# Performance work log

Hardware: AMD Instinct MI355X
Metric: run time of the kernel (lower is better)

## Reference

```python
import jax, jax.numpy as jnp
import numpy as np

B, S, D = 4, 2048, 1024   # batch, seq_len, input feature dim
H, E = 16, 64             # head_num, att_embedding_size; H*E = model dim


def setup_inputs() -> dict:
    key = jax.random.key(0)
    ks = jax.random.split(key, 9)
    std = 1.0 / np.sqrt(D)
    M = H * E
    return {
        "x": jax.random.normal(ks[0], (B, S, D), dtype=jnp.float32),
        "Wq": jax.random.normal(ks[1], (D, M), dtype=jnp.float32) * std,
        "bq": jnp.zeros((M,), dtype=jnp.float32),
        "Wk": jax.random.normal(ks[2], (D, M), dtype=jnp.float32) * std,
        "bk": jnp.zeros((M,), dtype=jnp.float32),
        "Wv": jax.random.normal(ks[3], (D, M), dtype=jnp.float32) * std,
        "bv": jnp.zeros((M,), dtype=jnp.float32),
        "Wr": jax.random.normal(ks[4], (D, M), dtype=jnp.float32) * std,
        "br": jnp.zeros((M,), dtype=jnp.float32),
    }


def reference(x, Wq, bq, Wk, bk, Wv, bv, Wr, br):
    # QKV dense layers with ReLU activation (as in the original Keras code)
    qw = jax.nn.relu(x @ Wq + bq)                      # [B,S,H*E]
    kw = jax.nn.relu(x @ Wk + bk)
    vw = jax.nn.relu(x @ Wv + bv)
    # split heads: [B,S,H,E] -> [B,H,S,E]
    qw = qw.reshape(B, S, H, E).transpose(0, 2, 1, 3)
    kw = kw.reshape(B, S, H, E).transpose(0, 2, 1, 3)
    vw = vw.reshape(B, S, H, E).transpose(0, 2, 1, 3)
    # unscaled attention (original has no 1/sqrt(d) scaling)
    a = jnp.einsum("bhqe,bhke->bhqk", qw, kw)          # [B,H,S,S]
    a = jax.nn.softmax(a, axis=-1)
    o = jnp.einsum("bhqk,bhke->bhqe", a, vw)           # [B,H,S,E]
    o = o.transpose(0, 2, 1, 3).reshape(B, S, H * E)
    # residual dense (no activation)
    o = o + (x @ Wr + br)
    return o
```

## Files before the change

### kernel.cpp

```cpp
#include <hip/hip_runtime.h>


typedef __bf16 bf16x8 __attribute__((ext_vector_type(8)));
typedef float  f32x4  __attribute__((ext_vector_type(4)));
typedef short  short8 __attribute__((ext_vector_type(8)));
typedef short  short4v __attribute__((ext_vector_type(4)));
typedef float  float4v __attribute__((ext_vector_type(4)));
typedef int    int4v  __attribute__((ext_vector_type(4)));

#define LOG2E 1.44269504088896f

__device__ __forceinline__ unsigned short f2bf(float f) {
  unsigned u = __builtin_bit_cast(unsigned, f);
  u += 0x7fffu + ((u >> 16) & 1u);
  return (unsigned short)(u >> 16);
}

__device__ __forceinline__ unsigned pack2(float lo, float hi) {
  __bf16 a = (__bf16)lo, b = (__bf16)hi;
  unsigned short ua = __builtin_bit_cast(unsigned short, a);
  unsigned short ub = __builtin_bit_cast(unsigned short, b);
  return (unsigned)ua | ((unsigned)ub << 16);
}

__global__ __launch_bounds__(256) void k_cvt_x(const float* __restrict__ x,
                                               short* __restrict__ Xb) {
  const size_t i = ((size_t)blockIdx.x * 256 + threadIdx.x) * 4;
  float4v f = *(const float4v*)(x + i);
  short4v o;
  o[0] = (short)f2bf(f[0]); o[1] = (short)f2bf(f[1]);
  o[2] = (short)f2bf(f[2]); o[3] = (short)f2bf(f[3]);
  *(short4v*)(Xb + i) = o;
}

__global__ __launch_bounds__(256) void k_cvt_w(const float* __restrict__ Wq,
                                               const float* __restrict__ Wk,
                                               const float* __restrict__ Wv,
                                               const float* __restrict__ Wr,
                                               short* __restrict__ Wc) {
  const int bid = blockIdx.x;
  const int w = bid >> 8;
  const int t = bid & 255;
  const int tr = t >> 4, tc = t & 15;
  const float* Ws = (w == 0) ? Wq : (w == 1) ? Wk : (w == 2) ? Wv : Wr;
  __shared__ float T[64][65];
  const int tx = threadIdx.x & 63, ty = threadIdx.x >> 6;
#pragma unroll
  for (int i = 0; i < 16; ++i)
    T[i * 4 + ty][tx] = Ws[(size_t)(tr * 64 + i * 4 + ty) * 1024 + tc * 64 + tx];
  __syncthreads();
#pragma unroll
  for (int i = 0; i < 16; ++i) {
    const int n = tc * 64 + i * 4 + ty;
    Wc[((size_t)w * 1024 + n) * 1024 + tr * 64 + tx] = (short)f2bf(T[tx][i * 4 + ty]);
  }
}

__global__ __launch_bounds__(256) void k_gemm(const short* __restrict__ Xb,
                                              const short* __restrict__ Wc,
                                              const float* __restrict__ bq,
                                              const float* __restrict__ bk2,
                                              const float* __restrict__ bv,
                                              const float* __restrict__ br,
                                              short* __restrict__ Qb,
                                              short* __restrict__ Kb,
                                              short* __restrict__ Vb,
                                              float* __restrict__ Out) {
  __shared__ short As[128 * 32];
  __shared__ short Bs[128 * 32];
  const int tid = threadIdx.x, wid = tid >> 6, lane = tid & 63;
  const int lr = lane & 15, hi = lane >> 4;
  const int bm = blockIdx.x & 63, bn = blockIdx.x >> 6;
  const int m0 = bm * 128, n0 = bn * 128;
  const int wr = wid >> 1, wc = wid & 1;

  f32x4 acc[4][4] = {};

  const int c0 = wid * 2;
  const int srow = lane >> 2;
  const int scol = (lane & 3) * 8;

  for (int k0 = 0; k0 < 1024; k0 += 32) {
    __syncthreads();
    const short* a0 = Xb + (size_t)(m0 + c0 * 16 + srow) * 1024 + k0 + scol;
    const short* a1 = Xb + (size_t)(m0 + (c0 + 1) * 16 + srow) * 1024 + k0 + scol;
    const short* b0 = Wc + (size_t)(n0 + c0 * 16 + srow) * 1024 + k0 + scol;
    const short* b1 = Wc + (size_t)(n0 + (c0 + 1) * 16 + srow) * 1024 + k0 + scol;
    __builtin_amdgcn_global_load_lds((const __attribute__((address_space(1))) void*)a0,
                                     (__attribute__((address_space(3))) void*)&As[c0 * 512], 16, 0, 0);
    __builtin_amdgcn_global_load_lds((const __attribute__((address_space(1))) void*)a1,
                                     (__attribute__((address_space(3))) void*)&As[(c0 + 1) * 512], 16, 0, 0);
    __builtin_amdgcn_global_load_lds((const __attribute__((address_space(1))) void*)b0,
                                     (__attribute__((address_space(3))) void*)&Bs[c0 * 512], 16, 0, 0);
    __builtin_amdgcn_global_load_lds((const __attribute__((address_space(1))) void*)b1,
                                     (__attribute__((address_space(3))) void*)&Bs[(c0 + 1) * 512], 16, 0, 0);
    __syncthreads();

    bf16x8 af[4], bfr[4];
#pragma unroll
    for (int i = 0; i < 4; ++i)
      af[i] = *(const bf16x8*)&As[(wr * 64 + i * 16 + lr) * 32 + hi * 8];
#pragma unroll
    for (int j = 0; j < 4; ++j)
      bfr[j] = *(const bf16x8*)&Bs[(wc * 64 + j * 16 + lr) * 32 + hi * 8];
#pragma unroll
    for (int i = 0; i < 4; ++i)
#pragma unroll
      for (int j = 0; j < 4; ++j)
        acc[i][j] = __builtin_amdgcn_mfma_f32_16x16x32_bf16(af[i], bfr[j], acc[i][j], 0, 0, 0);
  }

#pragma unroll
  for (int i = 0; i < 4; ++i) {
    const int mbase = m0 + wr * 64 + i * 16 + hi * 4;
#pragma unroll
    for (int j = 0; j < 4; ++j) {
      const int n = n0 + wc * 64 + j * 16 + lr;
      const float* bp = (n < 2048) ? (n < 1024 ? bq : bk2) : (n < 3072 ? bv : br);
      const float bias = bp[n & 1023];
#pragma unroll
      for (int r = 0; r < 4; ++r) {
        float v = acc[i][j][r] + bias;
        const int m = mbase + r;
        if (n < 3072) {
          v = fmaxf(v, 0.0f);
          const int which = n >> 10;
          const int nn = n & 1023, h = nn >> 6, e = nn & 63;
          short* dst = (which == 0) ? Qb : (which == 1) ? Kb : Vb;
          const int bb = m >> 11, ss = m & 2047;
          dst[(((size_t)bb * 16 + h) * 2048 + ss) * 64 + e] = (short)f2bf(v);
        } else {
          Out[(size_t)m * 1024 + (n - 3072)] = v;
        }
      }
    }
  }
}

__global__ __launch_bounds__(256) void k_tr_v(const short* __restrict__ Vb,
                                              short* __restrict__ Vt) {
  __shared__ short T[64][72];
  const int bh = blockIdx.x >> 5;
  const int s0 = (blockIdx.x & 31) * 64;
  const size_t base = (size_t)bh * 2048 * 64;
  const int t = threadIdx.x;
  const int sl = t >> 2, e0 = (t & 3) * 16;
  const short* src = Vb + base + (size_t)(s0 + sl) * 64 + e0;
  *(short8*)&T[sl][e0] = *(const short8*)src;
  *(short8*)&T[sl][e0 + 8] = *(const short8*)(src + 8);
  __syncthreads();
  const int el = t >> 2, sc0 = (t & 3) * 16;
  const int b32 = sc0 & ~31;
  const int s_off = sc0 & 31;
  short tmp[16];
#pragma unroll
  for (int j = 0; j < 16; ++j) {
    const int sig = s_off + j;
    const int key = ((sig & 4) ? 16 : 0) + ((sig >> 3) << 2) + (sig & 3);
    tmp[j] = T[b32 + key][el];
  }
  short* dst = Vt + base + (size_t)el * 2048 + s0 + sc0;
  *(short8*)dst = *(const short8*)&tmp[0];
  *(short8*)(dst + 8) = *(const short8*)&tmp[8];
}

__global__ __launch_bounds__(256, 4) void k_attn(const short* __restrict__ Qb,
                                                 const short* __restrict__ Kb,
                                                 const short* __restrict__ Vt,
                                                 float* __restrict__ Out) {
  __shared__ __align__(16) short smem[16384];
  char* const sb = (char*)smem;
  const int tid = threadIdx.x, wid = tid >> 6, lane = tid & 63;
  const int lr = lane & 15, hi = lane >> 4;
  const int bid = ((blockIdx.x & 7) << 7) | (blockIdx.x >> 3);
  const int bh = bid >> 4;
  const int q0 = (bid & 15) * 128;
  const size_t hb = (size_t)bh * (2048 * 64);

  bf16x8 aq[2][2];
#pragma unroll
  for (int g = 0; g < 2; ++g) {
    const short* qp = Qb + hb + (size_t)(q0 + wid * 32 + g * 16 + lr) * 64 + hi * 8;
    aq[g][0] = *(const bf16x8*)qp;
    aq[g][1] = *(const bf16x8*)(qp + 32);
  }

  f32x4 o[2][4] = {};
  float l_run[2] = {0.f, 0.f};

  const int swz = ((lane & 7) ^ (lane >> 3)) * 8;
  const int rlo = lane >> 3;
  const int wr0 = wid * 16;
  const short* kp0 = Kb + hb + (size_t)(wr0 + rlo) * 64 + swz;
  const short* kp1 = kp0 + 8 * 64;
  const short* vp0 = Vt + hb + (size_t)(wr0 + rlo) * 2048 + swz;
  const short* vp1 = vp0 + 8 * 2048;

  const int vb0 = (lr * 64 + ((hi ^ (lr & 7)) << 3)) * 2;
  const int vb1 = vb0 ^ 64;

#define GLL(SRC, LDSOFF)                                                                   \
  __builtin_amdgcn_global_load_lds((const __attribute__((address_space(1))) void*)(SRC),   \
      (__attribute__((address_space(3))) void*)(sb + (LDSOFF)), 16, 0, 0)

  GLL(kp0, wr0 * 128);
  GLL(kp1, wr0 * 128 + 1024);
  GLL(vp0, 16384 + wr0 * 128);
  GLL(vp1, 16384 + wr0 * 128 + 1024);
  kp0 += 4096; kp1 += 4096; vp0 += 64; vp1 += 64;

  for (int kt = 0; kt < 32; ++kt) {
    const int buf = kt & 1;
    if (kt < 31) {
      const int d = (buf ^ 1) * 8192 + wr0 * 128;
      GLL(kp0, d);
      GLL(kp1, d + 1024);
      GLL(vp0, 16384 + d);
      GLL(vp1, 16384 + d + 1024);
      kp0 += 4096; kp1 += 4096; vp0 += 64; vp1 += 64;
      asm volatile("s_waitcnt vmcnt(4)" ::: "memory");
    } else {
      asm volatile("s_waitcnt vmcnt(0)" ::: "memory");
    }
    __builtin_amdgcn_sched_barrier(0);
    __builtin_amdgcn_s_barrier();
    __builtin_amdgcn_sched_barrier(0);

    f32x4 s[2][4];
#pragma unroll
    for (int kc = 0; kc < 4; ++kc) {
      const bf16x8 kf0 = *(const bf16x8*)(sb + (vb0 + buf * 8192 + kc * 2048));
      const bf16x8 kf1 = *(const bf16x8*)(sb + (vb1 + buf * 8192 + kc * 2048));
      f32x4 t0 = __builtin_amdgcn_mfma_f32_16x16x32_bf16(kf0, aq[0][0], (f32x4){0.f, 0.f, 0.f, 0.f}, 0, 0, 0);
      s[0][kc] = __builtin_amdgcn_mfma_f32_16x16x32_bf16(kf1, aq[0][1], t0, 0, 0, 0);
      f32x4 t1 = __builtin_amdgcn_mfma_f32_16x16x32_bf16(kf0, aq[1][0], (f32x4){0.f, 0.f, 0.f, 0.f}, 0, 0, 0);
      s[1][kc] = __builtin_amdgcn_mfma_f32_16x16x32_bf16(kf1, aq[1][1], t1, 0, 0, 0);
    }

    int4v pw[2][2];
#pragma unroll
    for (int g = 0; g < 2; ++g) {
      float sum = 0.f;
#pragma unroll
      for (int kc = 0; kc < 4; ++kc) {
        const float p0 = __builtin_amdgcn_exp2f(s[g][kc][0] * LOG2E);
        const float p1 = __builtin_amdgcn_exp2f(s[g][kc][1] * LOG2E);
        const float p2 = __builtin_amdgcn_exp2f(s[g][kc][2] * LOG2E);
        const float p3 = __builtin_amdgcn_exp2f(s[g][kc][3] * LOG2E);
        sum += (p0 + p1) + (p2 + p3);
        pw[g][kc >> 1][(kc & 1) * 2] = (int)pack2(p0, p1);
        pw[g][kc >> 1][(kc & 1) * 2 + 1] = (int)pack2(p2, p3);
      }
      l_run[g] += sum;
    }

#pragma unroll
    for (int kk = 0; kk < 2; ++kk) {
      const bf16x8 pa0 = __builtin_bit_cast(bf16x8, pw[0][kk]);
      const bf16x8 pa1 = __builtin_bit_cast(bf16x8, pw[1][kk]);
      const int cb = (kk ? vb1 : vb0) + 16384 + buf * 8192;
#pragma unroll
      for (int et = 0; et < 4; ++et) {
        const bf16x8 vf = *(const bf16x8*)(sb + (cb + et * 2048));
        o[0][et] = __builtin_amdgcn_mfma_f32_16x16x32_bf16(vf, pa0, o[0][et], 0, 0, 0);
        o[1][et] = __builtin_amdgcn_mfma_f32_16x16x32_bf16(vf, pa1, o[1][et], 0, 0, 0);
      }
    }

    asm volatile("s_waitcnt lgkmcnt(0)" ::: "memory");
    __builtin_amdgcn_sched_barrier(0);
    __builtin_amdgcn_s_barrier();
    __builtin_amdgcn_sched_barrier(0);
  }

  float* Ep = (float*)smem + wid * 1088;
  const int b = bh >> 4, h = bh & 15;
  const int qr = lane >> 2, cc = lane & 3;
#pragma unroll
  for (int g = 0; g < 2; ++g) {
    float lt = l_run[g];
    lt += __shfl_xor(lt, 16);
    lt += __shfl_xor(lt, 32);
    const float inv = 1.0f / lt;
#pragma unroll
    for (int et = 0; et < 4; ++et) {
      f32x4 v = o[g][et] * inv;
      *(float4v*)&Ep[lr * 68 + et * 16 + hi * 4] = v;
    }
    asm volatile("s_waitcnt lgkmcnt(0)" ::: "memory");
    const size_t gb = ((size_t)b * 2048 + q0 + wid * 32 + g * 16 + qr) * 1024 + h * 64 + cc * 4;
#pragma unroll
    for (int i = 0; i < 4; ++i) {
      float4v v = *(const float4v*)&Ep[qr * 68 + cc * 4 + i * 16];
      float4v u = *(const float4v*)&Out[gb + i * 16];
      u += v;
      *(float4v*)&Out[gb + i * 16] = u;
    }
    asm volatile("s_waitcnt lgkmcnt(0)" ::: "memory");
  }
#undef GLL
}

extern "C" void kernel_launch(void* const* d_in, const int* in_sizes, int n_in,
                              void* d_out, int out_size, void* d_ws, size_t ws_size,
                              hipStream_t stream) {
  const float* x  = (const float*)d_in[0];
  const float* Wq = (const float*)d_in[1];
  const float* bq = (const float*)d_in[2];
  const float* Wk = (const float*)d_in[3];
  const float* bk = (const float*)d_in[4];
  const float* Wv = (const float*)d_in[5];
  const float* bv = (const float*)d_in[6];
  const float* Wr = (const float*)d_in[7];
  const float* br = (const float*)d_in[8];
  float* Out = (float*)d_out;

  char* ws = (char*)d_ws;
  short* Xb = (short*)(ws);
  short* Wc = (short*)(ws + (size_t)16 * 1024 * 1024);
  short* Qb = (short*)(ws + (size_t)24 * 1024 * 1024);
  short* Kb = (short*)(ws + (size_t)40 * 1024 * 1024);
  short* Vb = (short*)(ws + (size_t)56 * 1024 * 1024);
  short* Vt = (short*)(ws);

  k_cvt_x<<<8192, 256, 0, stream>>>(x, Xb);
  k_cvt_w<<<1024, 256, 0, stream>>>(Wq, Wk, Wv, Wr, Wc);
  k_gemm<<<2048, 256, 0, stream>>>(Xb, Wc, bq, bk, bv, br, Qb, Kb, Vb, Out);
  k_tr_v<<<2048, 256, 0, stream>>>(Vb, Vt);
  k_attn<<<1024, 256, 0, stream>>>(Qb, Kb, Vt, Out);
}
```

Before: 201.2 us.

## Fuse V transpose into GEMM epilogue and widen attention query tile

The GEMM epilogue now writes V directly in the transposed, key-permuted layout the attention kernel reads, so the separate transpose kernel and its extra read/write pass over V go away. The attention kernel now handles 256 query rows per block (64 per wave) instead of 128, so each K/V tile loaded into shared memory is reused by twice as many queries, and the grid halves to 512 blocks. MFMA sections are wrapped in s_setprio. In exchange, register pressure goes up (launch bounds drop to 2 blocks per CU), and the V stores from the GEMM become strided 8-byte scatters.

```diff
diff --git a/kernel.cpp b/kernel.cpp
--- a/kernel.cpp
+++ b/kernel.cpp
@@ -7,6 +7,7 @@
 typedef short  short4v __attribute__((ext_vector_type(4)));
 typedef float  float4v __attribute__((ext_vector_type(4)));
 typedef int    int4v  __attribute__((ext_vector_type(4)));
+typedef unsigned uint2v __attribute__((ext_vector_type(2)));
 
 #define LOG2E 1.44269504088896f
 
@@ -64,7 +65,7 @@
                                               const float* __restrict__ br,
                                               short* __restrict__ Qb,
                                               short* __restrict__ Kb,
-                                              short* __restrict__ Vb,
+                                              short* __restrict__ Vt,
                                               float* __restrict__ Out) {
   __shared__ short As[128 * 32];
   __shared__ short Bs[128 * 32];
@@ -113,58 +114,40 @@
 #pragma unroll
   for (int i = 0; i < 4; ++i) {
     const int mbase = m0 + wr * 64 + i * 16 + hi * 4;
+    const int bb = mbase >> 11, sbase = mbase & 2047;
 #pragma unroll
     for (int j = 0; j < 4; ++j) {
       const int n = n0 + wc * 64 + j * 16 + lr;
       const float* bp = (n < 2048) ? (n < 1024 ? bq : bk2) : (n < 3072 ? bv : br);
       const float bias = bp[n & 1023];
-#pragma unroll
-      for (int r = 0; r < 4; ++r) {
-        float v = acc[i][j][r] + bias;
-        const int m = mbase + r;
-        if (n < 3072) {
-          v = fmaxf(v, 0.0f);
-          const int which = n >> 10;
-          const int nn = n & 1023, h = nn >> 6, e = nn & 63;
-          short* dst = (which == 0) ? Qb : (which == 1) ? Kb : Vb;
-          const int bb = m >> 11, ss = m & 2047;
-          dst[(((size_t)bb * 16 + h) * 2048 + ss) * 64 + e] = (short)f2bf(v);
-        } else {
-          Out[(size_t)m * 1024 + (n - 3072)] = v;
-        }
+      float v[4];
+#pragma unroll
+      for (int r = 0; r < 4; ++r) v[r] = acc[i][j][r] + bias;
+
+      if (n < 2048) {
+        const int nn = n & 1023, h = nn >> 6, e = nn & 63;
+        short* dst = (n < 1024) ? Qb : Kb;
+#pragma unroll
+        for (int r = 0; r < 4; ++r)
+          dst[(((size_t)bb * 16 + h) * 2048 + sbase + r) * 64 + e] = (short)f2bf(fmaxf(v[r], 0.f));
+      } else if (n < 3072) {
+        const int nn = n & 1023, h = nn >> 6, e = nn & 63;
+        const int kq = sbase & 31;
+        const int Sp = (sbase & ~31) + ((kq >> 2) & 3) * 8 + (kq >> 4) * 4;
+        uint2v pv;
+        pv[0] = pack2(fmaxf(v[0], 0.f), fmaxf(v[1], 0.f));
+        pv[1] = pack2(fmaxf(v[2], 0.f), fmaxf(v[3], 0.f));
+        *(uint2v*)&Vt[(((size_t)bb * 16 + h) * 64 + e) * 2048 + Sp] = pv;
+      } else {
+#pragma unroll
+        for (int r = 0; r < 4; ++r)
+          Out[(size_t)(mbase + r) * 1024 + (n - 3072)] = v[r];
       }
     }
   }
 }
 
-__global__ __launch_bounds__(256) void k_tr_v(const short* __restrict__ Vb,
-                                              short* __restrict__ Vt) {
-  __shared__ short T[64][72];
-  const int bh = blockIdx.x >> 5;
-  const int s0 = (blockIdx.x & 31) * 64;
-  const size_t base = (size_t)bh * 2048 * 64;
-  const int t = threadIdx.x;
-  const int sl = t >> 2, e0 = (t & 3) * 16;
-  const short* src = Vb + base + (size_t)(s0 + sl) * 64 + e0;
-  *(short8*)&T[sl][e0] = *(const short8*)src;
-  *(short8*)&T[sl][e0 + 8] = *(const short8*)(src + 8);
-  __syncthreads();
-  const int el = t >> 2, sc0 = (t & 3) * 16;
-  const int b32 = sc0 & ~31;
-  const int s_off = sc0 & 31;
-  short tmp[16];
-#pragma unroll
-  for (int j = 0; j < 16; ++j) {
-    const int sig = s_off + j;
-    const int key = ((sig & 4) ? 16 : 0) + ((sig >> 3) << 2) + (sig & 3);
-    tmp[j] = T[b32 + key][el];
-  }
-  short* dst = Vt + base + (size_t)el * 2048 + s0 + sc0;
-  *(short8*)dst = *(const short8*)&tmp[0];
-  *(short8*)(dst + 8) = *(const short8*)&tmp[8];
-}
-
-__global__ __launch_bounds__(256, 4) void k_attn(const short* __restrict__ Qb,
+__global__ __launch_bounds__(256, 2) void k_attn(const short* __restrict__ Qb,
                                                  const short* __restrict__ Kb,
                                                  const short* __restrict__ Vt,
                                                  float* __restrict__ Out) {
@@ -172,21 +155,21 @@
   char* const sb = (char*)smem;
   const int tid = threadIdx.x, wid = tid >> 6, lane = tid & 63;
   const int lr = lane & 15, hi = lane >> 4;
-  const int bid = ((blockIdx.x & 7) << 7) | (blockIdx.x >> 3);
-  const int bh = bid >> 4;
-  const int q0 = (bid & 15) * 128;
+  const int bid = ((blockIdx.x & 7) << 6) | (blockIdx.x >> 3);
+  const int bh = bid >> 3;
+  const int q0 = (bid & 7) * 256;
   const size_t hb = (size_t)bh * (2048 * 64);
 
-  bf16x8 aq[2][2];
-#pragma unroll
-  for (int g = 0; g < 2; ++g) {
-    const short* qp = Qb + hb + (size_t)(q0 + wid * 32 + g * 16 + lr) * 64 + hi * 8;
+  bf16x8 aq[4][2];
+#pragma unroll
+  for (int g = 0; g < 4; ++g) {
+    const short* qp = Qb + hb + (size_t)(q0 + wid * 64 + g * 16 + lr) * 64 + hi * 8;
     aq[g][0] = *(const bf16x8*)qp;
     aq[g][1] = *(const bf16x8*)(qp + 32);
   }
 
-  f32x4 o[2][4] = {};
-  float l_run[2] = {0.f, 0.f};
+  f32x4 o[4][4] = {};
+  float l_run[4] = {0.f, 0.f, 0.f, 0.f};
 
   const int swz = ((lane & 7) ^ (lane >> 3)) * 8;
   const int rlo = lane >> 3;
@@ -226,20 +209,23 @@
     __builtin_amdgcn_s_barrier();
     __builtin_amdgcn_sched_barrier(0);
 
-    f32x4 s[2][4];
+    f32x4 s[4][4];
+    __builtin_amdgcn_s_setprio(1);
 #pragma unroll
     for (int kc = 0; kc < 4; ++kc) {
       const bf16x8 kf0 = *(const bf16x8*)(sb + (vb0 + buf * 8192 + kc * 2048));
       const bf16x8 kf1 = *(const bf16x8*)(sb + (vb1 + buf * 8192 + kc * 2048));
-      f32x4 t0 = __builtin_amdgcn_mfma_f32_16x16x32_bf16(kf0, aq[0][0], (f32x4){0.f, 0.f, 0.f, 0.f}, 0, 0, 0);
-      s[0][kc] = __builtin_amdgcn_mfma_f32_16x16x32_bf16(kf1, aq[0][1], t0, 0, 0, 0);
-      f32x4 t1 = __builtin_amdgcn_mfma_f32_16x16x32_bf16(kf0, aq[1][0], (f32x4){0.f, 0.f, 0.f, 0.f}, 0, 0, 0);
-      s[1][kc] = __builtin_amdgcn_mfma_f32_16x16x32_bf16(kf1, aq[1][1], t1, 0, 0, 0);
-    }
-
-    int4v pw[2][2];
-#pragma unroll
-    for (int g = 0; g < 2; ++g) {
+#pragma unroll
+      for (int g = 0; g < 4; ++g) {
+        f32x4 t = __builtin_amdgcn_mfma_f32_16x16x32_bf16(kf0, aq[g][0], (f32x4){0.f, 0.f, 0.f, 0.f}, 0, 0, 0);
+        s[g][kc] = __builtin_amdgcn_mfma_f32_16x16x32_bf16(kf1, aq[g][1], t, 0, 0, 0);
+      }
+    }
+    __builtin_amdgcn_s_setprio(0);
+
+    int4v pw[4][2];
+#pragma unroll
+    for (int g = 0; g < 4; ++g) {
       float sum = 0.f;
 #pragma unroll
       for (int kc = 0; kc < 4; ++kc) {
@@ -254,18 +240,20 @@
       l_run[g] += sum;
     }
 
+    __builtin_amdgcn_s_setprio(1);
 #pragma unroll
     for (int kk = 0; kk < 2; ++kk) {
-      const bf16x8 pa0 = __builtin_bit_cast(bf16x8, pw[0][kk]);
-      const bf16x8 pa1 = __builtin_bit_cast(bf16x8, pw[1][kk]);
       const int cb = (kk ? vb1 : vb0) + 16384 + buf * 8192;
 #pragma unroll
       for (int et = 0; et < 4; ++et) {
         const bf16x8 vf = *(const bf16x8*)(sb + (cb + et * 2048));
-        o[0][et] = __builtin_amdgcn_mfma_f32_16x16x32_bf16(vf, pa0, o[0][et], 0, 0, 0);
-        o[1][et] = __builtin_amdgcn_mfma_f32_16x16x32_bf16(vf, pa1, o[1][et], 0, 0, 0);
+#pragma unroll
+        for (int g = 0; g < 4; ++g)
+          o[g][et] = __builtin_amdgcn_mfma_f32_16x16x32_bf16(
+              vf, __builtin_bit_cast(bf16x8, pw[g][kk]), o[g][et], 0, 0, 0);
       }
     }
+    __builtin_amdgcn_s_setprio(0);
 
     asm volatile("s_waitcnt lgkmcnt(0)" ::: "memory");
     __builtin_amdgcn_sched_barrier(0);
@@ -277,7 +265,7 @@
   const int b = bh >> 4, h = bh & 15;
   const int qr = lane >> 2, cc = lane & 3;
 #pragma unroll
-  for (int g = 0; g < 2; ++g) {
+  for (int g = 0; g < 4; ++g) {
     float lt = l_run[g];
     lt += __shfl_xor(lt, 16);
     lt += __shfl_xor(lt, 32);
@@ -288,7 +276,7 @@
       *(float4v*)&Ep[lr * 68 + et * 16 + hi * 4] = v;
     }
     asm volatile("s_waitcnt lgkmcnt(0)" ::: "memory");
-    const size_t gb = ((size_t)b * 2048 + q0 + wid * 32 + g * 16 + qr) * 1024 + h * 64 + cc * 4;
+    const size_t gb = ((size_t)b * 2048 + q0 + wid * 64 + g * 16 + qr) * 1024 + h * 64 + cc * 4;
 #pragma unroll
     for (int i = 0; i < 4; ++i) {
       float4v v = *(const float4v*)&Ep[qr * 68 + cc * 4 + i * 16];
@@ -320,12 +308,10 @@
   short* Wc = (short*)(ws + (size_t)16 * 1024 * 1024);
   short* Qb = (short*)(ws + (size_t)24 * 1024 * 1024);
   short* Kb = (short*)(ws + (size_t)40 * 1024 * 1024);
-  short* Vb = (short*)(ws + (size_t)56 * 1024 * 1024);
-  short* Vt = (short*)(ws);
+  short* Vt = (short*)(ws + (size_t)56 * 1024 * 1024);
 
   k_cvt_x<<<8192, 256, 0, stream>>>(x, Xb);
   k_cvt_w<<<1024, 256, 0, stream>>>(Wq, Wk, Wv, Wr, Wc);
-  k_gemm<<<2048, 256, 0, stream>>>(Xb, Wc, bq, bk, bv, br, Qb, Kb, Vb, Out);
-  k_tr_v<<<2048, 256, 0, stream>>>(Vb, Vt);
-  k_attn<<<1024, 256, 0, stream>>>(Qb, Kb, Vt, Out);
-}
+  k_gemm<<<2048, 256, 0, stream>>>(Xb, Wc, bq, bk, bv, br, Qb, Kb, Vt, Out);
+  k_attn<<<512, 256, 0, stream>>>(Qb, Kb, Vt, Out);
+}
```

After: 189.2 us. 6.0% less time.
